# Kernel optimization log

Hardware: AMD Instinct MI355X
Metric: run time of the kernel (lower is better)

The kernel has to match this reference:

```python
import jax, jax.numpy as jnp
import numpy as np

N = 1_000_000   # mesh points
D_IN = 5        # scalar invariants
H = 128         # hidden width
L = 5           # hidden layers
NB = 10         # tensor bases

# t0 generator basis rows (flattened 3x3 deviatoric diag tensors)
T01 = np.array([-1/3, 0, 0, 0, 1/6, 0, 0, 0, 1/6], dtype=np.float32)
T02 = np.array([1/6, 0, 0, 0, -1/3, 0, 0, 0, 1/6], dtype=np.float32)
T03 = np.array([1/6, 0, 0, 0, 1/6, 0, 0, 0, -1/3], dtype=np.float32)


def _linear_params(k, fan_in, fan_out):
    # xavier_uniform_ with gain=1.0, bias filled with 0.01 (as in init_w_and_b)
    limit = float(np.sqrt(6.0 / (fan_in + fan_out)))
    W = jax.random.uniform(k, (fan_in, fan_out), jnp.float32, -limit, limit)
    b = jnp.full((fan_out,), 0.01, jnp.float32)
    return W, b


def setup_inputs() -> dict:
    key = jax.random.key(0)
    ks = jax.random.split(key, 16)
    x = jax.random.normal(ks[0], (N, D_IN), jnp.float32)
    tb = jax.random.normal(ks[1], (N, NB, 9), jnp.float32)
    inp = {"x": x, "tb": tb}
    dims = [D_IN] + [H] * L
    for i in range(L):
        W, b = _linear_params(ks[2 + i], dims[i], dims[i + 1])
        inp[f"W{i+1}"] = W
        inp[f"b{i+1}"] = b
    inp["Wc"], inp["bc"] = _linear_params(ks[2 + L], H, NB)
    inp["Wg1"], inp["bg1"] = _linear_params(ks[3 + L], H, 1)
    inp["Wg2"], inp["bg2"] = _linear_params(ks[4 + L], H, 1)
    inp["Wg3"], inp["bg3"] = _linear_params(ks[5 + L], H, 1)
    return inp


def reference(x, tb, W1, b1, W2, b2, W3, b3, W4, b4, W5, b5,
              Wc, bc, Wg1, bg1, Wg2, bg2, Wg3, bg3):
    h = x
    for W, b in ((W1, b1), (W2, b2), (W3, b3), (W4, b4), (W5, b5)):
        h = jax.nn.relu(h @ W + b)          # [N, H]
    coeffs = h @ Wc + bc                     # [N, NB]
    g1 = h @ Wg1 + bg1                       # [N, 1]
    g2 = h @ Wg2 + bg2
    g3 = h @ Wg3 + bg3
    t0 = g1 * jnp.asarray(T01) + g2 * jnp.asarray(T02) + g3 * jnp.asarray(T03)  # [N, 9]
    # batched tensor-basis contraction replacing the per-point double loop
    bij = t0 + jnp.einsum('nt,ntc->nc', coeffs, tb)  # [N, 9]
    return bij
```

## Files before the change

kernel.cpp:

```cpp
#include <hip/hip_runtime.h>
#include <stdint.h>


#define NPTS   1000000
#define TPB    256
#define NBLKS  256
#define PTILE  256
#define NT     ((NPTS + PTILE - 1) / PTILE)

typedef uint32_t u32;
typedef __attribute__((ext_vector_type(4)))  u32   u32x4;
typedef __attribute__((ext_vector_type(8)))  short s16x8;
typedef __attribute__((ext_vector_type(16))) float f32x16;
typedef __attribute__((ext_vector_type(4), aligned(4))) float f32x4u;

#define WS_L(l)   ((l)*65536)
#define WS_TAIL   262144
#define WS_W1     (262144 + 8192)
#define WS_BIAS   (262144 + 12288)

#define LDS_BUF0   0
#define LDS_BUF1   65536
#define LDS_HEADS  131072
#define LDS_W1     (131072 + 8192)
#define LDS_BIAS   (131072 + 12288)
#define LDS_TOTAL  147456

#define MFMA(a,b,c) __builtin_amdgcn_mfma_f32_32x32x16_bf16((a),(b),(c),0,0,0)
#define BC16(v)     __builtin_bit_cast(s16x8, (v))

__device__ __forceinline__ u32 cvtpk(float lo, float hi) {
    u32 r;
    asm("v_cvt_pk_bf16_f32 %0, %1, %2" : "=v"(r) : "v"(lo), "v"(hi));
    return r;
}
__device__ __forceinline__ float lo2f(u32 p){ return __builtin_bit_cast(float, p << 16); }
__device__ __forceinline__ float hi2f(u32 p){ return __builtin_bit_cast(float, p & 0xffff0000u); }
__device__ __forceinline__ uint16_t f2bf(float f) {
    u32 u = __builtin_bit_cast(u32, f);
    return (uint16_t)((u + 0x7fffu + ((u >> 16) & 1u)) >> 16);
}
__device__ __forceinline__ float b2f(uint16_t h){ return __builtin_bit_cast(float, (u32)h << 16); }

__device__ __forceinline__ void stageN(const char* g, char* l, int tid, int nbytes) {
    const int w = tid >> 6, ln = tid & 63;
    const char* gp = g + w*1024 + ln*16;
    char* lp = l + w*1024;
    #pragma unroll
    for (int i = 0; i < 16; ++i) {
        if (i*4096 >= nbytes) break;
        __builtin_amdgcn_global_load_lds(
            (const __attribute__((address_space(1))) uint32_t*)(gp + i*4096),
            (__attribute__((address_space(3))) uint32_t*)(lp + i*4096), 16, 0, 0);
    }
}

extern "C" __global__ void __launch_bounds__(256)
tbnn_prep(const float* __restrict__ W1, const float* __restrict__ b1,
          const float* __restrict__ W2, const float* __restrict__ b2,
          const float* __restrict__ W3, const float* __restrict__ b3,
          const float* __restrict__ W4, const float* __restrict__ b4,
          const float* __restrict__ W5, const float* __restrict__ b5,
          const float* __restrict__ Wc, const float* __restrict__ bc,
          const float* __restrict__ Wg1,const float* __restrict__ bg1,
          const float* __restrict__ Wg2,const float* __restrict__ bg2,
          const float* __restrict__ Wg3,const float* __restrict__ bg3,
          char* __restrict__ ws)
{
    int idx = blockIdx.x*256 + threadIdx.x;
    if (idx < 65536) {
        int l = idx >> 14, r = idx & 16383, ifc = r >> 7, of = r & 127;
        const float* Wt = (l==0)?W2:(l==1)?W3:(l==2)?W4:W5;
        float w = Wt[ifc*128 + of];
        uint16_t hb = f2bf(w);
        uint16_t lb = f2bf(w - b2f(hb));
        char* row = ws + WS_L(l) + of*512;
        int o = (2*ifc) ^ ((of&15)<<4);
        *(uint16_t*)(row + o)       = hb;
        *(uint16_t*)(row + 256 + o) = lb;
    } else if (idx < 65536 + 2048) {
        int j = idx - 65536, of = j >> 7, ifc = j & 127;
        float v = 0.f;
        if      (of < 10)  v = Wc[ifc*10 + of];
        else if (of == 10) v = Wg1[ifc];
        else if (of == 11) v = Wg2[ifc];
        else if (of == 12) v = Wg3[ifc];
        uint16_t hb = f2bf(v);
        uint16_t lb = f2bf(v - b2f(hb));
        char* row = ws + WS_TAIL + of*512;
        int o = (2*ifc) ^ ((of&15)<<4);
        *(uint16_t*)(row + o)       = hb;
        *(uint16_t*)(row + 256 + o) = lb;
    } else if (idx < 65536 + 2048 + 128) {
        int of = idx - (65536 + 2048);
        uint16_t* dst = (uint16_t*)(ws + WS_W1 + of*32);
        #pragma unroll
        for (int s = 0; s < 5; ++s) {
            float w = W1[s*128 + of];
            uint16_t hb = f2bf(w);
            dst[s]      = hb;
            dst[6 + s]  = f2bf(w - b2f(hb));
            dst[11 + s] = hb;
        }
        dst[5] = f2bf(b1[of]);
    } else if (idx < 65536 + 2048 + 128 + 544) {
        int j = idx - (65536 + 2048 + 128);
        float v = 0.f;
        if (j < 512) {
            int l = j >> 7, of = j & 127;
            const float* bt = (l==0)?b2:(l==1)?b3:(l==2)?b4:b5;
            v = bt[of];
        } else {
            int of = j - 512;
            if      (of < 10)  v = bc[of];
            else if (of == 10) v = bg1[0];
            else if (of == 11) v = bg2[0];
            else if (of == 12) v = bg3[0];
        }
        *(uint16_t*)(ws + WS_BIAS + j*2) = f2bf(v);
    }
}

extern "C" __global__ void __launch_bounds__(TPB, 1)
tbnn_main(const float* __restrict__ x, const float* __restrict__ tb,
          const char* __restrict__ ws, float* __restrict__ out)
{
    extern __shared__ char smem[];
    const int tid  = threadIdx.x;
    const int wave = tid >> 6;
    const int lane = tid & 63;
    const int col  = lane & 31;
    const int hi   = lane >> 5;
    const int sm   = (col & 15) << 4;
    const int hib  = hi * 16;

    stageN(ws + WS_TAIL, smem + LDS_HEADS, tid, 16384);
    stageN(ws + WS_L(0), smem + LDS_BUF0,  tid, 65536);
    stageN(ws + WS_L(1), smem + LDS_BUF1,  tid, 65536);
    __syncthreads();

    u32x4 Bc; Bc[0] = hi ? 0u : 0x00003F80u; Bc[1]=0u; Bc[2]=0u; Bc[3]=0u;
    f32x16 zf;
    #pragma unroll
    for (int i = 0; i < 16; ++i) zf[i] = 0.f;

    f32x16 accA[4], accB[4];
    u32x4  BAh[8], BAl[8], BBh[8], BBl[8];

    auto convert = [&](const f32x16 (&ac)[4], u32x4 (&BH)[8], u32x4 (&BL)[8]) {
        #pragma unroll
        for (int ot = 0; ot < 4; ++ot) {
            f32x16 a = ac[ot];
            #pragma unroll
            for (int h2 = 0; h2 < 2; ++h2) {
                float e0 = fmaxf(a[8*h2+0], 0.f), e1 = fmaxf(a[8*h2+1], 0.f);
                float e2 = fmaxf(a[8*h2+2], 0.f), e3 = fmaxf(a[8*h2+3], 0.f);
                float e4 = fmaxf(a[8*h2+4], 0.f), e5 = fmaxf(a[8*h2+5], 0.f);
                float e6 = fmaxf(a[8*h2+6], 0.f), e7 = fmaxf(a[8*h2+7], 0.f);
                u32 h01 = cvtpk(e0,e1), h23 = cvtpk(e2,e3);
                u32 h45 = cvtpk(e4,e5), h67 = cvtpk(e6,e7);
                u32 l01 = cvtpk(e0 - lo2f(h01), e1 - hi2f(h01));
                u32 l23 = cvtpk(e2 - lo2f(h23), e3 - hi2f(h23));
                u32 l45 = cvtpk(e4 - lo2f(h45), e5 - hi2f(h45));
                u32 l67 = cvtpk(e6 - lo2f(h67), e7 - hi2f(h67));
                auto sh1 = __builtin_amdgcn_permlane32_swap(h01, h45, false, false);
                auto sh2 = __builtin_amdgcn_permlane32_swap(h23, h67, false, false);
                u32x4 fh; fh[0]=sh1[0]; fh[1]=sh2[0]; fh[2]=sh1[1]; fh[3]=sh2[1];
                BH[2*ot+h2] = fh;
                auto sl1 = __builtin_amdgcn_permlane32_swap(l01, l45, false, false);
                auto sl2 = __builtin_amdgcn_permlane32_swap(l23, l67, false, false);
                u32x4 fl; fl[0]=sl1[0]; fl[1]=sl2[0]; fl[2]=sl1[1]; fl[3]=sl2[1];
                BL[2*ot+h2] = fl;
            }
        }
    };

    auto l1 = [&](int p, f32x16 (&dst)[4]) {
        float x0=0.f,x1=0.f,x2=0.f,x3=0.f,x4=0.f;
        if (p < NPTS) {
            const float* xp = x + (size_t)p*5;
            f32x4u v = *(const f32x4u*)xp;
            x0=v.x; x1=v.y; x2=v.z; x3=v.w; x4=xp[4];
        }
        float h0 = lo2f(cvtpk(x0,x0)), l0 = x0 - h0;
        float h1 = lo2f(cvtpk(x1,x1)), l1v = x1 - h1;
        float h2 = lo2f(cvtpk(x2,x2)), l2 = x2 - h2;
        float h3 = lo2f(cvtpk(x3,x3)), l3 = x3 - h3;
        float h4 = lo2f(cvtpk(x4,x4)), l4 = x4 - h4;
        u32x4 Bx;
        if (hi == 0) {
            Bx[0] = cvtpk(h0,h1); Bx[1] = cvtpk(h2,h3);
            Bx[2] = cvtpk(h4,1.0f); Bx[3] = cvtpk(h0,h1);
        } else {
            Bx[0] = cvtpk(h2,h3); Bx[1] = cvtpk(h4,l0);
            Bx[2] = cvtpk(l1v,l2); Bx[3] = cvtpk(l3,l4);
        }
        #pragma unroll
        for (int ot = 0; ot < 4; ++ot) {
            u32x4 Av = *(const u32x4*)(smem + LDS_W1 + (ot*32+col)*32 + hib);
            dst[ot] = MFMA(BC16(Av), BC16(Bx), zf);
        }
    };

    auto kloop = [&](const char* wb) {
        #pragma unroll
        for (int k = 0; k < 8; ++k) {
            int so = (k*32 + hib) ^ sm;
            const char* rp = wb + col*512 + so;
            #pragma unroll
            for (int ot = 0; ot < 4; ++ot) {
                u32x4 H = *(const u32x4*)(rp + ot*16384);
                u32x4 L = *(const u32x4*)(rp + ot*16384 + 256);
                s16x8 h = BC16(H), lo = BC16(L);
                accA[ot] = MFMA(h,  BC16(BAl[k]), (k==0)?zf:accA[ot]);
                accB[ot] = MFMA(h,  BC16(BBl[k]), (k==0)?zf:accB[ot]);
                accA[ot] = MFMA(h,  BC16(BAh[k]), accA[ot]);
                accB[ot] = MFMA(h,  BC16(BBh[k]), accB[ot]);
                accA[ot] = MFMA(lo, BC16(BAh[k]), accA[ot]);
                accB[ot] = MFMA(lo, BC16(BBh[k]), accB[ot]);
            }
        }
    };
    auto biask = [&](int lc) {
        #pragma unroll
        for (int ot = 0; ot < 4; ++ot) {
            u32 bw = (u32)*(const uint16_t*)(smem + LDS_BIAS + (lc*128 + ot*32 + col)*2);
            u32x4 Ab; Ab[0] = hi ? 0u : bw; Ab[1]=0u; Ab[2]=0u; Ab[3]=0u;
            accA[ot] = MFMA(BC16(Ab), BC16(Bc), accA[ot]);
            accB[ot] = MFMA(BC16(Ab), BC16(Bc), accB[ot]);
        }
    };

    auto headsBoth = [&](f32x16& h6a, f32x16& h6b) {
        #pragma unroll
        for (int k = 0; k < 8; ++k) {
            int so = (k*32 + hib) ^ sm;
            const char* rp = smem + LDS_HEADS + (col&15)*512;
            u32x4 HH = *(const u32x4*)(rp + so);
            u32x4 HL = *(const u32x4*)(rp + 256 + so);
            s16x8 h = BC16(HH), lo = BC16(HL);
            h6a = MFMA(h,  BC16(BAl[k]), (k==0)?zf:h6a);
            h6b = MFMA(h,  BC16(BBl[k]), (k==0)?zf:h6b);
            h6a = MFMA(h,  BC16(BAh[k]), h6a);
            h6b = MFMA(h,  BC16(BBh[k]), h6b);
            h6a = MFMA(lo, BC16(BAh[k]), h6a);
            h6b = MFMA(lo, BC16(BBh[k]), h6b);
        }
        u32 bw = (u32)*(const uint16_t*)(smem + LDS_BIAS + (512 + col)*2);
        u32x4 Ab; Ab[0] = hi ? 0u : bw; Ab[1]=0u; Ab[2]=0u; Ab[3]=0u;
        h6a = MFMA(BC16(Ab), BC16(Bc), h6a);
        h6b = MFMA(BC16(Ab), BC16(Bc), h6b);
    };

    auto contraction = [&](int p, f32x16 c) {
        if (p >= NPTS) return;
        const float* tbp = tb + (size_t)p*90;
        const float sixth = 0.16666666666666666f;
        const float third = 0.3333333333333333f;
        float s[9];
        if (hi == 0) {
            float g1 = c[6], g2 = c[7];
            s[0] = -g1*third + g2*sixth;
            s[4] =  g1*sixth - g2*third;
            s[8] =  g1*sixth + g2*sixth;
        } else {
            float g3 = c[4];
            s[0] =  g3*sixth;
            s[4] =  g3*sixth;
            s[8] = -g3*third;
        }
        s[1]=s[2]=s[3]=s[5]=s[6]=s[7]=0.f;
        #pragma unroll
        for (int j = 0; j < 4; ++j) {
            int trow = (hi ? 4 : 0) + j;
            float cf = c[j];
            const float* r = tbp + trow*9;
            f32x4u r0 = *(const f32x4u*)(r);
            f32x4u r1 = *(const f32x4u*)(r + 4);
            float r8 = r[8];
            s[0] += cf*r0.x; s[1] += cf*r0.y; s[2] += cf*r0.z; s[3] += cf*r0.w;
            s[4] += cf*r1.x; s[5] += cf*r1.y; s[6] += cf*r1.z; s[7] += cf*r1.w;
            s[8] += cf*r8;
        }
        if (hi == 0) {
            #pragma unroll
            for (int j = 4; j < 6; ++j) {
                int trow = 4 + j;
                float cf = c[j];
                const float* r = tbp + trow*9;
                f32x4u r0 = *(const f32x4u*)(r);
                f32x4u r1 = *(const f32x4u*)(r + 4);
                float r8 = r[8];
                s[0] += cf*r0.x; s[1] += cf*r0.y; s[2] += cf*r0.z; s[3] += cf*r0.w;
                s[4] += cf*r1.x; s[5] += cf*r1.y; s[6] += cf*r1.z; s[7] += cf*r1.w;
                s[8] += cf*r8;
            }
        }
        #pragma unroll
        for (int j = 0; j < 9; ++j) {
            u32 uv = __builtin_bit_cast(u32, s[j]);
            auto rr = __builtin_amdgcn_permlane32_swap(uv, uv, false, false);
            s[j] = __builtin_bit_cast(float, (u32)rr[0]) + __builtin_bit_cast(float, (u32)rr[1]);
        }
        if (hi == 0) {
            float* op = out + (size_t)p*9;
            f32x4u o0, o1;
            o0.x=s[0]; o0.y=s[1]; o0.z=s[2]; o0.w=s[3];
            o1.x=s[4]; o1.y=s[5]; o1.z=s[6]; o1.w=s[7];
            *(f32x4u*)op       = o0;
            *(f32x4u*)(op + 4) = o1;
            op[8] = s[8];
        }
    };

    for (int t = blockIdx.x; t < NT; t += gridDim.x) {
        const int pA = t*PTILE + wave*64 + col;
        const int pB = pA + 32;

        l1(pA, accA); convert(accA, BAh, BAl);
        l1(pB, accB); convert(accB, BBh, BBl);

        kloop(smem + LDS_BUF0); biask(0);
        convert(accA, BAh, BAl); convert(accB, BBh, BBl);
        __syncthreads();
        stageN(ws + WS_L(2), smem + LDS_BUF0, tid, 65536);

        kloop(smem + LDS_BUF1); biask(1);
        convert(accA, BAh, BAl); convert(accB, BBh, BBl);
        __syncthreads();
        stageN(ws + WS_L(3), smem + LDS_BUF1, tid, 65536);

        kloop(smem + LDS_BUF0); biask(2);
        convert(accA, BAh, BAl); convert(accB, BBh, BBl);
        __syncthreads();
        stageN(ws + WS_L(0), smem + LDS_BUF0, tid, 65536);

        kloop(smem + LDS_BUF1); biask(3);
        convert(accA, BAh, BAl); convert(accB, BBh, BBl);
        __syncthreads();
        stageN(ws + WS_L(1), smem + LDS_BUF1, tid, 65536);

        f32x16 h6a, h6b;
        headsBoth(h6a, h6b);
        contraction(pA, h6a);
        contraction(pB, h6b);
    }
    __syncthreads();
}

extern "C" void kernel_launch(void* const* d_in, const int* in_sizes, int n_in,
                              void* d_out, int out_size, void* d_ws, size_t ws_size,
                              hipStream_t stream) {
    (void)in_sizes; (void)n_in; (void)out_size; (void)ws_size;
    char* ws = (char*)d_ws;
    hipLaunchKernelGGL(tbnn_prep, dim3(267), dim3(256), 0, stream,
        (const float*)d_in[2],  (const float*)d_in[3],
        (const float*)d_in[4],  (const float*)d_in[5],
        (const float*)d_in[6],  (const float*)d_in[7],
        (const float*)d_in[8],  (const float*)d_in[9],
        (const float*)d_in[10], (const float*)d_in[11],
        (const float*)d_in[12], (const float*)d_in[13],
        (const float*)d_in[14], (const float*)d_in[15],
        (const float*)d_in[16], (const float*)d_in[17],
        (const float*)d_in[18], (const float*)d_in[19],
        ws);
    (void)hipFuncSetAttribute((const void*)tbnn_main,
                              hipFuncAttributeMaxDynamicSharedMemorySize, LDS_TOTAL);
    hipLaunchKernelGGL(tbnn_main, dim3(NBLKS), dim3(TPB), LDS_TOTAL, stream,
        (const float*)d_in[0], (const float*)d_in[1], ws, (float*)d_out);
}
```

Measured before the change: 429.1 us.

## Process point groups A and B sequentially per layer to overlap convert and staging

The hidden-layer k-loop now handles the two 32-point groups one after another instead of interleaving them. This lets group A's bf16 split/convert overlap group B's MFMAs, and group B's convert happen after the barrier and weight staging. Within each k step the four output-tile loads are issued first, then the MFMAs are grouped by operand. The heads computation splits the dependent accumulation chain across two accumulators (even/odd k) and sums them. Each group re-reads the weight tile from LDS, which doubles LDS read traffic, and register pressure may change.

```diff
diff --git a/kernel.cpp b/kernel.cpp
--- a/kernel.cpp
+++ b/kernel.cpp
@@ -202,54 +202,62 @@
         }
     };
 
-    auto kloop = [&](const char* wb) {
+    auto kloopG = [&](const char* wb, f32x16 (&ac)[4],
+                      const u32x4 (&BH)[8], const u32x4 (&BL)[8]) {
         #pragma unroll
         for (int k = 0; k < 8; ++k) {
             int so = (k*32 + hib) ^ sm;
             const char* rp = wb + col*512 + so;
+            u32x4 H[4], L[4];
             #pragma unroll
             for (int ot = 0; ot < 4; ++ot) {
-                u32x4 H = *(const u32x4*)(rp + ot*16384);
-                u32x4 L = *(const u32x4*)(rp + ot*16384 + 256);
-                s16x8 h = BC16(H), lo = BC16(L);
-                accA[ot] = MFMA(h,  BC16(BAl[k]), (k==0)?zf:accA[ot]);
-                accB[ot] = MFMA(h,  BC16(BBl[k]), (k==0)?zf:accB[ot]);
-                accA[ot] = MFMA(h,  BC16(BAh[k]), accA[ot]);
-                accB[ot] = MFMA(h,  BC16(BBh[k]), accB[ot]);
-                accA[ot] = MFMA(lo, BC16(BAh[k]), accA[ot]);
-                accB[ot] = MFMA(lo, BC16(BBh[k]), accB[ot]);
+                H[ot] = *(const u32x4*)(rp + ot*16384);
+                L[ot] = *(const u32x4*)(rp + ot*16384 + 256);
             }
-        }
-    };
-    auto biask = [&](int lc) {
+            s16x8 bl = BC16(BL[k]), bh = BC16(BH[k]);
+            #pragma unroll
+            for (int ot = 0; ot < 4; ++ot)
+                ac[ot] = MFMA(BC16(H[ot]), bl, (k==0)?zf:ac[ot]);
+            #pragma unroll
+            for (int ot = 0; ot < 4; ++ot)
+                ac[ot] = MFMA(BC16(H[ot]), bh, ac[ot]);
+            #pragma unroll
+            for (int ot = 0; ot < 4; ++ot)
+                ac[ot] = MFMA(BC16(L[ot]), bh, ac[ot]);
+        }
+    };
+    auto biasG = [&](int lc, f32x16 (&ac)[4]) {
         #pragma unroll
         for (int ot = 0; ot < 4; ++ot) {
             u32 bw = (u32)*(const uint16_t*)(smem + LDS_BIAS + (lc*128 + ot*32 + col)*2);
             u32x4 Ab; Ab[0] = hi ? 0u : bw; Ab[1]=0u; Ab[2]=0u; Ab[3]=0u;
-            accA[ot] = MFMA(BC16(Ab), BC16(Bc), accA[ot]);
-            accB[ot] = MFMA(BC16(Ab), BC16(Bc), accB[ot]);
-        }
-    };
-
-    auto headsBoth = [&](f32x16& h6a, f32x16& h6b) {
+            ac[ot] = MFMA(BC16(Ab), BC16(Bc), ac[ot]);
+        }
+    };
+
+    auto headsG = [&](const u32x4 (&BH)[8], const u32x4 (&BL)[8]) -> f32x16 {
+        f32x16 hA, hB;
+        const char* rp = smem + LDS_HEADS + (col&15)*512;
         #pragma unroll
         for (int k = 0; k < 8; ++k) {
             int so = (k*32 + hib) ^ sm;
-            const char* rp = smem + LDS_HEADS + (col&15)*512;
             u32x4 HH = *(const u32x4*)(rp + so);
             u32x4 HL = *(const u32x4*)(rp + 256 + so);
             s16x8 h = BC16(HH), lo = BC16(HL);
-            h6a = MFMA(h,  BC16(BAl[k]), (k==0)?zf:h6a);
-            h6b = MFMA(h,  BC16(BBl[k]), (k==0)?zf:h6b);
-            h6a = MFMA(h,  BC16(BAh[k]), h6a);
-            h6b = MFMA(h,  BC16(BBh[k]), h6b);
-            h6a = MFMA(lo, BC16(BAh[k]), h6a);
-            h6b = MFMA(lo, BC16(BBh[k]), h6b);
+            if (k & 1) {
+                hB = MFMA(h,  BC16(BL[k]), (k==1)?zf:hB);
+                hB = MFMA(h,  BC16(BH[k]), hB);
+                hB = MFMA(lo, BC16(BH[k]), hB);
+            } else {
+                hA = MFMA(h,  BC16(BL[k]), (k==0)?zf:hA);
+                hA = MFMA(h,  BC16(BH[k]), hA);
+                hA = MFMA(lo, BC16(BH[k]), hA);
+            }
         }
         u32 bw = (u32)*(const uint16_t*)(smem + LDS_BIAS + (512 + col)*2);
         u32x4 Ab; Ab[0] = hi ? 0u : bw; Ab[1]=0u; Ab[2]=0u; Ab[3]=0u;
-        h6a = MFMA(BC16(Ab), BC16(Bc), h6a);
-        h6b = MFMA(BC16(Ab), BC16(Bc), h6b);
+        hA = MFMA(BC16(Ab), BC16(Bc), hA);
+        return hA + hB;
     };
 
     auto contraction = [&](int p, f32x16 c) {
@@ -313,38 +321,34 @@
         }
     };
 
+    #define LAYER(lc, BUFOFF, WSNEXT)                                   \
+        kloopG(smem + (BUFOFF), accA, BAh, BAl); biasG(lc, accA);       \
+        convert(accA, BAh, BAl);     \
+        kloopG(smem + (BUFOFF), accB, BBh, BBl); biasG(lc, accB);       \
+        __syncthreads();             \
+        stageN(ws + (WSNEXT), smem + (BUFOFF), tid, 65536);             \
+        convert(accB, BBh, BBl);
+
     for (int t = blockIdx.x; t < NT; t += gridDim.x) {
         const int pA = t*PTILE + wave*64 + col;
         const int pB = pA + 32;
 
-        l1(pA, accA); convert(accA, BAh, BAl);
-        l1(pB, accB); convert(accB, BBh, BBl);
-
-        kloop(smem + LDS_BUF0); biask(0);
-        convert(accA, BAh, BAl); convert(accB, BBh, BBl);
-        __syncthreads();
-        stageN(ws + WS_L(2), smem + LDS_BUF0, tid, 65536);
-
-        kloop(smem + LDS_BUF1); biask(1);
-        convert(accA, BAh, BAl); convert(accB, BBh, BBl);
-        __syncthreads();
-        stageN(ws + WS_L(3), smem + LDS_BUF1, tid, 65536);
-
-        kloop(smem + LDS_BUF0); biask(2);
-        convert(accA, BAh, BAl); convert(accB, BBh, BBl);
-        __syncthreads();
-        stageN(ws + WS_L(0), smem + LDS_BUF0, tid, 65536);
-
-        kloop(smem + LDS_BUF1); biask(3);
-        convert(accA, BAh, BAl); convert(accB, BBh, BBl);
-        __syncthreads();
-        stageN(ws + WS_L(1), smem + LDS_BUF1, tid, 65536);
-
-        f32x16 h6a, h6b;
-        headsBoth(h6a, h6b);
+        l1(pA, accA);
+        convert(accA, BAh, BAl);
+        l1(pB, accB);
+        convert(accB, BBh, BBl);
+
+        LAYER(0, LDS_BUF0, WS_L(2));
+        LAYER(1, LDS_BUF1, WS_L(3));
+        LAYER(2, LDS_BUF0, WS_L(0));
+        LAYER(3, LDS_BUF1, WS_L(1));
+
+        f32x16 h6a = headsG(BAh, BAl);
+        f32x16 h6b = headsG(BBh, BBl);
         contraction(pA, h6a);
         contraction(pB, h6b);
     }
+    #undef LAYER
     __syncthreads();
 }
 
```

Result: slower. 458.4 us (+6.8%).
